# Kernel optimization log

Measured on AMD Instinct MI355X. Metric: run time of the kernel, lower is better.

Reference implementation:

```python
import jax, jax.numpy as jnp
import numpy as np

HIDDEN_DIM = 400
STACK_DEPTH = 32
BATCH = 1
SEQ_LEN = 8192


def setup_inputs() -> dict:
    key = jax.random.key(0)
    k1, k2, k3 = jax.random.split(key, 3)
    hidden_state = jax.random.normal(k1, (BATCH, SEQ_LEN, HIDDEN_DIM), dtype=jnp.float32)
    # action_predictor: nn.Linear(hidden_dim, 3)
    W_ap = jax.random.normal(k2, (3, HIDDEN_DIM), dtype=jnp.float32) * 0.05
    b_ap = jnp.zeros((3,), dtype=jnp.float32)
    # D: nn.Parameter(torch.randn(1, hidden_dim))
    D = jax.random.normal(k3, (1, HIDDEN_DIM), dtype=jnp.float32)
    return {"hidden_state": hidden_state, "W_ap": W_ap, "b_ap": b_ap, "D": D}


def reference(hidden_state, W_ap, b_ap, D):
    # hidden_state: [B, T, H]
    B, T, H = hidden_state.shape
    # Per-step action probabilities (computed for all t at once): [B, T, 3]
    probs = jax.nn.softmax(jnp.einsum('bth,ah->bta', hidden_state, W_ap) + b_ap, axis=-1)
    # push value: sigmoid(D . h_t), scalar per (b, t) (well-defined at B=1)
    pv = jax.nn.sigmoid(jnp.einsum('bth,h->bt', hidden_state, D[0]))  # [B, T]
    push = jnp.transpose(probs[..., 0])   # [T, B]
    pop_ = jnp.transpose(probs[..., 1])   # [T, B]
    noop = jnp.transpose(probs[..., 2])   # [T, B]
    pv_t = jnp.transpose(pv)              # [T, B]

    stack0 = jnp.zeros((B, STACK_DEPTH, H), dtype=hidden_state.dtype)

    # Net effect of the two aliased in-place shifts (snapshot semantics):
    #   s2[0] = s[1]; s2[i] = s[i] for i >= 1
    # then stack[0] = push*push_val + pop*s2[1] + noop*s2[0]
    #               = push*push_val + (pop+noop)*s[1]
    def step(stack, xs):
        pu, po, no, v = xs  # each [B]
        s1 = stack[:, 1, :]  # [B, H]
        new_top = (pu * v)[:, None] + (po + no)[:, None] * s1  # [B, H]
        new_stack = stack.at[:, 0, :].set(new_top)
        return new_stack, new_stack

    _, stacks = jax.lax.scan(step, stack0, (push, pop_, noop, pv_t))  # [T, B, D, H]
    return jnp.transpose(stacks, (1, 0, 2, 3))  # [B, T, D, H]
```

## Files before the change

### kernel.cpp

```cpp
#include <hip/hip_runtime.h>

#define HDIM   400
#define TLEN   8192
#define DEPTH  32
#define SLICE4 ((DEPTH * HDIM) / 4)
#define ROW4   (HDIM / 4)
#define BLOCK  256
#define NCHUNK (SLICE4 / BLOCK)

typedef float floatx4 __attribute__((ext_vector_type(4)));

__global__ __launch_bounds__(BLOCK) void fused_kernel(
    const float* __restrict__ hs,
    const float* __restrict__ W,
    const float* __restrict__ b,
    const float* __restrict__ D,
    floatx4* __restrict__ out)
{
    const int t    = blockIdx.x;
    const int tid  = threadIdx.x;
    const int wave = tid >> 6;
    const int lane = tid & 63;

    const float* __restrict__ x = hs + (size_t)t * HDIM;
    floatx4* __restrict__ o = out + (size_t)t * SLICE4;
    const floatx4 z4 = (floatx4){0.f, 0.f, 0.f, 0.f};

    const float h0  = x[tid];
    const float w00 = W[tid];
    const float w10 = W[HDIM + tid];
    const float w20 = W[2 * HDIM + tid];
    const float d0  = D[tid];
    const int   i2  = tid + BLOCK;
    const bool  has2 = (i2 < HDIM);
    float h1 = 0.f, w01 = 0.f, w11 = 0.f, w21 = 0.f, d1 = 0.f;
    if (has2) {
        h1  = x[i2];
        w01 = W[i2];
        w11 = W[HDIM + i2];
        w21 = W[2 * HDIM + i2];
        d1  = D[i2];
    }

    if (tid >= ROW4) __builtin_nontemporal_store(z4, &o[tid]);
    #pragma unroll
    for (int k = 1; k < NCHUNK; ++k)
        __builtin_nontemporal_store(z4, &o[tid + k * BLOCK]);
    if (tid < SLICE4 - NCHUNK * BLOCK)
        __builtin_nontemporal_store(z4, &o[tid + NCHUNK * BLOCK]);

    float a0 = fmaf(h0, w00, h1 * w01);
    float a1 = fmaf(h0, w10, h1 * w11);
    float a2 = fmaf(h0, w20, h1 * w21);
    float ad = fmaf(h0, d0,  h1 * d1);

    #pragma unroll
    for (int off = 32; off > 0; off >>= 1) {
        a0 += __shfl_xor(a0, off);
        a1 += __shfl_xor(a1, off);
        a2 += __shfl_xor(a2, off);
        ad += __shfl_xor(ad, off);
    }

    __shared__ float red[4][BLOCK / 64];
    if (lane == 0) {
        red[0][wave] = a0; red[1][wave] = a1;
        red[2][wave] = a2; red[3][wave] = ad;
    }
    __syncthreads();
    a0 = red[0][0] + red[0][1] + red[0][2] + red[0][3];
    a1 = red[1][0] + red[1][1] + red[1][2] + red[1][3];
    a2 = red[2][0] + red[2][1] + red[2][2] + red[2][3];
    ad = red[3][0] + red[3][1] + red[3][2] + red[3][3];

    const float l0 = a0 + b[0];
    const float l1 = a1 + b[1];
    const float l2 = a2 + b[2];
    const float m  = fmaxf(l0, fmaxf(l1, l2));
    const float e0 = __expf(l0 - m);
    const float e1 = __expf(l1 - m);
    const float e2 = __expf(l2 - m);
    const float v  = (e0 / (e0 + e1 + e2)) / (1.f + __expf(-ad));

    if (tid < ROW4) {
        const floatx4 v4 = (floatx4){v, v, v, v};
        __builtin_nontemporal_store(v4, &o[tid]);
    }
}

extern "C" void kernel_launch(void* const* d_in, const int* in_sizes, int n_in,
                              void* d_out, int out_size, void* d_ws, size_t ws_size,
                              hipStream_t stream) {
    const float* hs = (const float*)d_in[0];
    const float* W  = (const float*)d_in[1];
    const float* b  = (const float*)d_in[2];
    const float* D  = (const float*)d_in[3];
    floatx4* out = (floatx4*)d_out;

    fused_kernel<<<TLEN, BLOCK, 0, stream>>>(hs, W, b, D, out);
}
```

Baseline: 429.9 us.

## Zero output with hipMemsetAsync and compute row-0 values per wavefront

Zero-filling of the ~420MB output moves from per-block nontemporal stores to a hipMemsetAsync. A small kernel then writes only row 0 of each time step. That kernel maps one wavefront per time step, so the cross-wave shared-memory reduction and barrier go away. The cost is an extra launch, and row 0 is written twice: once by the memset, then again with normal rather than nontemporal stores.

```diff
diff --git a/kernel.cpp b/kernel.cpp
--- a/kernel.cpp
+++ b/kernel.cpp
@@ -3,56 +3,34 @@
 #define HDIM   400
 #define TLEN   8192
 #define DEPTH  32
-#define SLICE4 ((DEPTH * HDIM) / 4)
+#define SLICE  (DEPTH * HDIM)
+#define SLICE4 (SLICE / 4)
 #define ROW4   (HDIM / 4)
 #define BLOCK  256
-#define NCHUNK (SLICE4 / BLOCK)
 
 typedef float floatx4 __attribute__((ext_vector_type(4)));
 
-__global__ __launch_bounds__(BLOCK) void fused_kernel(
+__global__ __launch_bounds__(BLOCK) void val_row0_kernel(
     const float* __restrict__ hs,
     const float* __restrict__ W,
     const float* __restrict__ b,
     const float* __restrict__ D,
     floatx4* __restrict__ out)
 {
-    const int t    = blockIdx.x;
-    const int tid  = threadIdx.x;
-    const int wave = tid >> 6;
-    const int lane = tid & 63;
+    const int wave = threadIdx.x >> 6;
+    const int lane = threadIdx.x & 63;
+    const int t = blockIdx.x * (BLOCK / 64) + wave;
 
     const float* __restrict__ x = hs + (size_t)t * HDIM;
-    floatx4* __restrict__ o = out + (size_t)t * SLICE4;
-    const floatx4 z4 = (floatx4){0.f, 0.f, 0.f, 0.f};
 
-    const float h0  = x[tid];
-    const float w00 = W[tid];
-    const float w10 = W[HDIM + tid];
-    const float w20 = W[2 * HDIM + tid];
-    const float d0  = D[tid];
-    const int   i2  = tid + BLOCK;
-    const bool  has2 = (i2 < HDIM);
-    float h1 = 0.f, w01 = 0.f, w11 = 0.f, w21 = 0.f, d1 = 0.f;
-    if (has2) {
-        h1  = x[i2];
-        w01 = W[i2];
-        w11 = W[HDIM + i2];
-        w21 = W[2 * HDIM + i2];
-        d1  = D[i2];
+    float a0 = 0.f, a1 = 0.f, a2 = 0.f, ad = 0.f;
+    for (int i = lane; i < HDIM; i += 64) {
+        const float h = x[i];
+        a0 = fmaf(h, W[i],            a0);
+        a1 = fmaf(h, W[HDIM + i],     a1);
+        a2 = fmaf(h, W[2 * HDIM + i], a2);
+        ad = fmaf(h, D[i],            ad);
     }
-
-    if (tid >= ROW4) __builtin_nontemporal_store(z4, &o[tid]);
-    #pragma unroll
-    for (int k = 1; k < NCHUNK; ++k)
-        __builtin_nontemporal_store(z4, &o[tid + k * BLOCK]);
-    if (tid < SLICE4 - NCHUNK * BLOCK)
-        __builtin_nontemporal_store(z4, &o[tid + NCHUNK * BLOCK]);
-
-    float a0 = fmaf(h0, w00, h1 * w01);
-    float a1 = fmaf(h0, w10, h1 * w11);
-    float a2 = fmaf(h0, w20, h1 * w21);
-    float ad = fmaf(h0, d0,  h1 * d1);
 
     #pragma unroll
     for (int off = 32; off > 0; off >>= 1) {
@@ -61,17 +39,6 @@
         a2 += __shfl_xor(a2, off);
         ad += __shfl_xor(ad, off);
     }
-
-    __shared__ float red[4][BLOCK / 64];
-    if (lane == 0) {
-        red[0][wave] = a0; red[1][wave] = a1;
-        red[2][wave] = a2; red[3][wave] = ad;
-    }
-    __syncthreads();
-    a0 = red[0][0] + red[0][1] + red[0][2] + red[0][3];
-    a1 = red[1][0] + red[1][1] + red[1][2] + red[1][3];
-    a2 = red[2][0] + red[2][1] + red[2][2] + red[2][3];
-    ad = red[3][0] + red[3][1] + red[3][2] + red[3][3];
 
     const float l0 = a0 + b[0];
     const float l1 = a1 + b[1];
@@ -82,10 +49,10 @@
     const float e2 = __expf(l2 - m);
     const float v  = (e0 / (e0 + e1 + e2)) / (1.f + __expf(-ad));
 
-    if (tid < ROW4) {
-        const floatx4 v4 = (floatx4){v, v, v, v};
-        __builtin_nontemporal_store(v4, &o[tid]);
-    }
+    floatx4* __restrict__ o = out + (size_t)t * SLICE4;
+    const floatx4 v4 = (floatx4){v, v, v, v};
+    o[lane] = v4;
+    if (lane < ROW4 - 64) o[64 + lane] = v4;
 }
 
 extern "C" void kernel_launch(void* const* d_in, const int* in_sizes, int n_in,
@@ -97,5 +64,7 @@
     const float* D  = (const float*)d_in[3];
     floatx4* out = (floatx4*)d_out;
 
-    fused_kernel<<<TLEN, BLOCK, 0, stream>>>(hs, W, b, D, out);
+    hipMemsetAsync(d_out, 0, (size_t)TLEN * SLICE * sizeof(float), stream);
+
+    val_row0_kernel<<<TLEN / (BLOCK / 64), BLOCK, 0, stream>>>(hs, W, b, D, out);
 }
```

Result: faster. 420.1 us (-2.3%).
